# Performance work log

Measured on AMD Instinct MI355X. Metric: run time of the kernel, lower is better.

## Reference

```python
import jax, jax.numpy as jnp
import numpy as np

IMG = 224   # img_size
K = 8       # num_bands
E = 256     # embed_dim


def _radial_masks(size, k):
    # Faithful to torch _create_radial_masks: center = size//2, max_r = size/sqrt(2)
    center = size // 2
    y, x = jnp.meshgrid(jnp.arange(size), jnp.arange(size), indexing='ij')
    r = jnp.sqrt(((x - center) ** 2 + (y - center) ** 2).astype(jnp.float32))
    max_r = size / np.sqrt(2.0)
    step = np.float32(max_r / k)
    i = jnp.arange(k, dtype=jnp.float32)[:, None, None]
    masks = ((r[None] >= step * i) & (r[None] < step * (i + 1.0))).astype(jnp.float32)
    return masks  # [K, H, W]


def setup_inputs() -> dict:
    key = jax.random.key(0)
    ks = jax.random.split(key, 3)
    x = jax.random.normal(ks[0], (64, 3, IMG, IMG), dtype=jnp.float32)
    W1 = jax.random.normal(ks[1], (3, E), dtype=jnp.float32) * 0.3
    b1 = jnp.zeros((E,), jnp.float32)
    gamma = jnp.ones((E,), jnp.float32)
    beta = jnp.zeros((E,), jnp.float32)
    W2 = jax.random.normal(ks[2], (E, E), dtype=jnp.float32) * (1.0 / np.sqrt(E))
    b2 = jnp.zeros((E,), jnp.float32)
    return {"x": x, "W1": W1, "b1": b1, "gamma": gamma, "beta": beta, "W2": W2, "b2": b2}


def reference(x, W1, b1, gamma, beta, W2, b2):
    masks = _radial_masks(IMG, K)                    # [K,H,W], binary, non-overlapping
    x_gray = x.mean(axis=1)                          # [B,H,W]
    fft = jnp.fft.fftshift(jnp.fft.fft2(x_gray), axes=(-2, -1))
    mag = jnp.log1p(jnp.abs(fft))                    # log(1+|F|)
    mu = mag.mean(axis=(1, 2), keepdims=True)
    sd = jnp.std(mag, axis=(1, 2), keepdims=True, ddof=1) + 1e-6  # torch .std is unbiased
    magn = (mag - mu) / sd                           # [B,H,W]

    msum = masks.sum(axis=(1, 2))                    # [K], true mask pixel counts
    mask_sums = msum + 1e-6
    s1 = jnp.einsum('bhw,khw->bk', magn, masks)      # per-band sum
    s2 = jnp.einsum('bhw,khw->bk', magn * magn, masks)
    means = s1 / mask_sums
    # sum((magn - means)^2 * mask) = s2 - 2*means*s1 + means^2 * msum  (exact expansion)
    var_num = s2 - 2.0 * means * s1 + (means ** 2) * msum
    stds = jnp.sqrt(var_num / mask_sums + 1e-6)
    # masked_fill(mask==0, -1e9) then amax over H,W
    maxs = jnp.max(jnp.where(masks[None] > 0, magn[:, None], -1e9), axis=(2, 3))

    feats = jnp.stack([means, stds, maxs], axis=-1)  # [B,K,3]
    h = feats @ W1 + b1                              # [B,K,E]
    hm = h.mean(axis=-1, keepdims=True)
    hv = h.var(axis=-1, keepdims=True)
    h = (h - hm) / jnp.sqrt(hv + 1e-5) * gamma + beta  # LayerNorm, eps=1e-5
    h = jax.nn.relu(h)
    return h @ W2 + b2                               # [B,K,E]
```

## Files before the change

kernel.cpp:

```cpp
#include <hip/hip_runtime.h>
#include <math.h>

#define IMG 224
#define NPIX 50176
#define BATCH 64
#define EDIM 256

typedef _Float16 f16;
typedef __attribute__((ext_vector_type(8))) _Float16 f16x8;
typedef __attribute__((ext_vector_type(4))) _Float16 f16x4;
typedef __attribute__((ext_vector_type(4))) float f32x4;
typedef unsigned int u32;


__global__ __launch_bounds__(256) void gemmA_kernel(const float* __restrict__ x,
                                                    f16* __restrict__ B2t,
                                                    f16* __restrict__ W2h,
                                                    u32* __restrict__ statsz) {
  __shared__ float T[224];
  __shared__ f16 As[2][32][64];
  __shared__ f16 Bs[2][256][64];
  int m0 = blockIdx.x * 32;
  int tid = threadIdx.x;
  int lane = tid & 63, wid = tid >> 6;

  if (blockIdx.x == 0) {
#pragma unroll
    for (int i = 0; i < 9; ++i) {
      int idx = i * 256 + tid;
      if (idx < 2176) statsz[idx] = 0u;
    }
  }

  int arow = tid >> 3;
  int aseg = tid & 7;
  int am = m0 + arow;
  int ab = am / 224, ah = am - ab * 224;
  const float* px = x + (size_t)ab * 3 * NPIX + ah * IMG;
  int s0 = aseg ^ (arow & 7);

  f32x4 xlA[3][2], xlB[3][2];
  f32x4 acc[2][4];
#pragma unroll
  for (int i = 0; i < 2; ++i)
#pragma unroll
    for (int j = 0; j < 4; ++j) acc[i][j] = (f32x4){0.f, 0.f, 0.f, 0.f};

  auto issueA = [&](f32x4 (&xl)[3][2], int t) {
    int kb = t * 64 + aseg * 8;
    if (kb < 224) {
#pragma unroll
      for (int c = 0; c < 3; ++c) {
        xl[c][0] = *(const f32x4*)(px + c * NPIX + kb);
        xl[c][1] = *(const f32x4*)(px + c * NPIX + kb + 4);
      }
    }
  };
  auto writeA = [&](f32x4 (&xl)[3][2], int t, int bufi) {
    int kb = t * 64 + aseg * 8;
    f16x8 h0;
    if (kb < 224) {
#pragma unroll
      for (int j = 0; j < 8; ++j) {
        int q = j >> 2, r = j & 3;
        h0[j] = (f16)((xl[0][q][r] + xl[1][q][r] + xl[2][q][r]) * (1.0f / 3.0f));
      }
    } else {
#pragma unroll
      for (int j = 0; j < 8; ++j) h0[j] = (f16)0.f;
    }
    *(f16x8*)&As[bufi][arow][s0 * 8] = h0;
  };
  auto computeB = [&](int bufi, int t) {
    int row = tid;
    int v = (row < 113) ? row : row - 113;
    u32 off = (row < 113) ? 0u : 56u;
    u32 idx0 = ((u32)(t * 64) * (u32)v + off) % 224u;
    u32 idxm = (idx0 >= (u32)v) ? idx0 - (u32)v : idx0 + 224u - (u32)v;
    float cur = T[idx0];
    float prev = T[idxm];
    float k2c = 2.0f * T[v];
#pragma unroll
    for (int g = 0; g < 8; ++g) {
      f16x8 hv;
#pragma unroll
      for (int j = 0; j < 8; ++j) {
        hv[j] = (f16)cur;
        float nxt = __builtin_fmaf(k2c, cur, -prev);
        prev = cur; cur = nxt;
      }
      *(f16x8*)&Bs[bufi][row][(g ^ (row & 7)) * 8] = hv;
    }
  };
  auto mfmaStep = [&](int bufi) {
#pragma unroll
    for (int kk = 0; kk < 2; ++kk) {
      f16x8 af[2], bfr[4];
#pragma unroll
      for (int mi = 0; mi < 2; ++mi) {
        int row = mi * 16 + (lane & 15);
        int slot = (kk * 4 + (lane >> 4)) ^ (row & 7);
        af[mi] = *(const f16x8*)&As[bufi][row][slot * 8];
      }
#pragma unroll
      for (int nj = 0; nj < 4; ++nj) {
        int row = wid * 64 + nj * 16 + (lane & 15);
        int slot = (kk * 4 + (lane >> 4)) ^ (row & 7);
        bfr[nj] = *(const f16x8*)&Bs[bufi][row][slot * 8];
      }
#pragma unroll
      for (int mi = 0; mi < 2; ++mi)
#pragma unroll
        for (int nj = 0; nj < 4; ++nj)
          acc[mi][nj] = __builtin_amdgcn_mfma_f32_16x16x32_f16(
              af[mi], bfr[nj], acc[mi][nj], 0, 0, 0);
    }
  };

  issueA(xlA, 0);
  if (tid < 224) T[tid] = cospif((float)tid / 112.0f);
  issueA(xlB, 1);
  __syncthreads();
  computeB(0, 0);

  asm volatile("s_waitcnt vmcnt(6)" ::: "memory");
  writeA(xlA, 0, 0);
  asm volatile("s_waitcnt lgkmcnt(0)" ::: "memory");
  __builtin_amdgcn_s_barrier();
  issueA(xlA, 2);
  computeB(1, 1);
  mfmaStep(0);
  __builtin_amdgcn_s_barrier();
  asm volatile("s_waitcnt vmcnt(6)" ::: "memory");
  writeA(xlB, 1, 1);
  asm volatile("s_waitcnt lgkmcnt(0)" ::: "memory");
  __builtin_amdgcn_s_barrier();
  issueA(xlB, 3);
  computeB(0, 2);
  mfmaStep(1);
  __builtin_amdgcn_s_barrier();
  asm volatile("s_waitcnt vmcnt(6)" ::: "memory");
  writeA(xlA, 2, 0);
  asm volatile("s_waitcnt lgkmcnt(0)" ::: "memory");
  __builtin_amdgcn_s_barrier();
  computeB(1, 3);
  mfmaStep(0);
  __builtin_amdgcn_s_barrier();
  asm volatile("s_waitcnt vmcnt(0)" ::: "memory");
  writeA(xlB, 3, 1);
  asm volatile("s_waitcnt lgkmcnt(0)" ::: "memory");
  __builtin_amdgcn_s_barrier();
  mfmaStep(1);

  int nbase = wid * 64;
#pragma unroll
  for (int mi = 0; mi < 2; ++mi) {
#pragma unroll
    for (int nj = 0; nj < 4; ++nj) {
      int c = nbase + nj * 16 + (lane & 15);
      if (c >= 226) continue;
      int m = m0 + mi * 16 + ((lane >> 4) << 2);
      int b = m / 224;
      int h = m - b * 224;
      int v = c, kb = h;
      if (c >= 113) { v = c - 113; kb = 224 + h; }
      size_t off = (size_t)(b * 128 + v) * 448 + kb;
      f32x4 y = acc[mi][nj];
      f16x4 hv;
#pragma unroll
      for (int r = 0; r < 4; ++r) hv[r] = (f16)y[r];
      *(f16x4*)&B2t[off] = hv;
    }
  }

  {
    int r = blockIdx.x;
    int u = r >> 1;
    bool imrow = r & 1;
#pragma unroll
    for (int pass = 0; pass < 2; ++pass) {
      int k = pass * 256 + tid;
      if (k < 448) {
        bool kim = k >= 224;
        int kk = kim ? k - 224 : k;
        int m = (u * kk) % 224;
        float mf = (float)m / 112.0f;
        float c = cospif(mf), s = sinpif(mf);
        float val = imrow ? (kim ? c : -s) : (kim ? s : c);
        W2h[(size_t)r * 448 + k] = (f16)val;
      }
    }
  }
}

__global__ __launch_bounds__(256) void gemmB_kernel(const f16* __restrict__ W2h,
                                                    const f16* __restrict__ B2t,
                                                    float* __restrict__ stats) {
  __shared__ f16 As[64][64];
  __shared__ f16 Bs[128][64];
  int b = blockIdx.x;
  int m0 = blockIdx.y * 64;
  int tid = threadIdx.x;
  int lane = tid & 63, wid = tid >> 6;
  int wr = wid >> 1, wc = wid & 1;
  const f16* Ap = W2h + (size_t)m0 * 448;
  const f16* Bp = B2t + (size_t)b * 128 * 448;

  int srow = lane >> 3;
  int sk8 = (lane & 7) ^ srow;

  f32x4 acc[2][4];
#pragma unroll
  for (int i = 0; i < 2; ++i)
#pragma unroll
    for (int j = 0; j < 4; ++j) acc[i][j] = (f32x4){0.f, 0.f, 0.f, 0.f};

  auto stage_load = [&](f16x8 (&tmp)[6], int t) {
    int k0 = t * 64;
#pragma unroll
    for (int ci = 0; ci < 6; ++ci) {
      int c = wid * 6 + ci;
      const f16* src = (c < 8)
          ? Ap + (size_t)(c * 8 + srow) * 448 + k0 + sk8 * 8
          : Bp + (size_t)((c - 8) * 8 + srow) * 448 + k0 + sk8 * 8;
      tmp[ci] = *(const f16x8*)src;
    }
  };
  auto stage_write = [&](f16x8 (&tmp)[6]) {
#pragma unroll
    for (int ci = 0; ci < 6; ++ci) {
      int c = wid * 6 + ci;
      f16* dst = (c < 8) ? (&As[0][0] + c * 512 + lane * 8)
                         : (&Bs[0][0] + (c - 8) * 512 + lane * 8);
      *(f16x8*)dst = tmp[ci];
    }
  };
  auto mfmaStep = [&]() {
#pragma unroll
    for (int kk = 0; kk < 2; ++kk) {
      f16x8 af[2], bfr[4];
#pragma unroll
      for (int mi = 0; mi < 2; ++mi) {
        int row = wr * 32 + mi * 16 + (lane & 15);
        int slot = (kk * 4 + (lane >> 4)) ^ (row & 7);
        af[mi] = *(const f16x8*)&As[row][slot * 8];
      }
#pragma unroll
      for (int nj = 0; nj < 4; ++nj) {
        int row = wc * 64 + nj * 16 + (lane & 15);
        int slot = (kk * 4 + (lane >> 4)) ^ (row & 7);
        bfr[nj] = *(const f16x8*)&Bs[row][slot * 8];
      }
#pragma unroll
      for (int mi = 0; mi < 2; ++mi)
#pragma unroll
        for (int nj = 0; nj < 4; ++nj)
          acc[mi][nj] = __builtin_amdgcn_mfma_f32_16x16x32_f16(
              af[mi], bfr[nj], acc[mi][nj], 0, 0, 0);
    }
  };
  auto step = [&](f16x8 (&curT)[6], f16x8 (&nxtT)[6], int t, bool last) {
    stage_write(curT);
    __syncthreads();
    if (!last) stage_load(nxtT, t + 1);
    mfmaStep();
    __syncthreads();
  };

  f16x8 tA[6], tB[6];
  stage_load(tA, 0);
  step(tA, tB, 0, false);
  step(tB, tA, 1, false);
  step(tA, tB, 2, false);
  step(tB, tA, 3, false);
  step(tA, tB, 4, false);
  step(tB, tA, 5, false);
  step(tA, tA, 6, true);

  int rbase = m0 + wr * 32;
  const float step_ = (float)(158.39191898578665 / 8.0);
  float gsum = 0.f, gsq = 0.f;
  float s1[8] = {0}, s2[8] = {0}, cnt[8] = {0};
  float mx[8] = {0, 0, 0, 0, 0, 0, 0, 0};

#pragma unroll
  for (int mi = 0; mi < 2; ++mi) {
#pragma unroll
    for (int nj = 0; nj < 4; ++nj) {
      int n = wc * 64 + nj * 16 + (lane & 15);
      if (n >= 113) continue;
      float wgt = (n >= 1 && n <= 111) ? 2.f : 1.f;
      float dx2 = (float)(n * n);
      int rr = rbase + mi * 16 + ((lane >> 4) << 2);
      f32x4 f = acc[mi][nj];
#pragma unroll
      for (int p = 0; p < 2; ++p) {
        int u = (rr >> 1) + p;
        float re = f[2 * p], im = f[2 * p + 1];
        float mv = log1pf(sqrtf(re * re + im * im));
        int a = (u <= 111) ? u : 224 - u;
        float r = sqrtf((float)(a * a) + dx2);
        int bd = 255;
#pragma unroll
        for (int k = 0; k < 8; k++) {
          float lo = step_ * (float)k;
          float hi = step_ * (float)(k + 1);
          if (r >= lo && r < hi) bd = k;
        }
        float wm = wgt * mv;
        gsum += wm;
        gsq += wm * mv;
#pragma unroll
        for (int k = 0; k < 8; k++) {
          bool m = (bd == k);
          s1[k] += m ? wm : 0.f;
          s2[k] += m ? wm * mv : 0.f;
          cnt[k] += m ? wgt : 0.f;
          mx[k] = m ? fmaxf(mx[k], mv) : mx[k];
        }
      }
    }
  }

  float vals[34];
  vals[0] = gsum; vals[1] = gsq;
#pragma unroll
  for (int k = 0; k < 8; k++) {
    vals[2 + k] = s1[k]; vals[10 + k] = s2[k]; vals[18 + k] = mx[k]; vals[26 + k] = cnt[k];
  }
#pragma unroll
  for (int i = 0; i < 34; i++) {
    float v = vals[i];
    const bool isMax = (i >= 18 && i < 26);
#pragma unroll
    for (int off = 32; off > 0; off >>= 1) {
      float o = __shfl_down(v, off);
      v = isMax ? fmaxf(v, o) : (v + o);
    }
    vals[i] = v;
  }
  float* red = (float*)&As[0][0];
  if ((tid & 63) == 0) {
#pragma unroll
    for (int i = 0; i < 34; i++) red[wid * 34 + i] = vals[i];
  }
  __syncthreads();
  if (tid < 34) {
    bool isMax = (tid >= 18 && tid < 26);
    float v = red[tid];
#pragma unroll
    for (int ww = 1; ww < 4; ww++) {
      float o = red[ww * 34 + tid];
      v = isMax ? fmaxf(v, o) : (v + o);
    }
    if (isMax)
      atomicMax((u32*)&stats[b * 34 + tid], __float_as_uint(v));
    else
      atomicAdd(&stats[b * 34 + tid], v);
  }
}

__global__ __launch_bounds__(256) void mlp_kernel(const float* __restrict__ stats,
                                                  const float* __restrict__ W1,
                                                  const float* __restrict__ b1,
                                                  const float* __restrict__ gamma,
                                                  const float* __restrict__ beta,
                                                  const float* __restrict__ W2m,
                                                  const float* __restrict__ b2,
                                                  float* __restrict__ out) {
  int blk = blockIdx.x;
  int b = blk >> 2;
  int k0 = (blk & 3) * 2;
  int e = threadIdx.x;
  int lane = e & 63, wave = e >> 6;

  __shared__ float st[34];
  if (e < 34) st[e] = stats[b * 34 + e];
  __syncthreads();

  const float N = (float)NPIX;
  float mu = st[0] / N;
  float varg = fmaxf(st[1] - N * mu * mu, 0.0f) / (N - 1.0f);
  float sd = sqrtf(varg) + 1e-6f;

  float g_e = gamma[e], bt_e = beta[e], b1_e = b1[e];
  float w1a = W1[e], w1b = W1[EDIM + e], w1c = W1[2 * EDIM + e];

  float h[2];
#pragma unroll
  for (int q = 0; q < 2; ++q) {
    int k = k0 + q;
    float s1r = st[2 + k], s2r = st[10 + k], mxr = st[18 + k], cntk = st[26 + k];
    float ms = cntk + 1e-6f;
    float s1n = (s1r - mu * cntk) / sd;
    float s2n = (s2r - 2.0f * mu * s1r + mu * mu * cntk) / (sd * sd);
    float mean_k = s1n / ms;
    float var_num = s2n - 2.0f * mean_k * s1n + mean_k * mean_k * cntk;
    float std_k = sqrtf(var_num / ms + 1e-6f);
    float max_k = (mxr - mu) / sd;
    h[q] = mean_k * w1a + std_k * w1b + max_k * w1c + b1_e;
  }

  float v4[4] = {h[0], h[0] * h[0], h[1], h[1] * h[1]};
#pragma unroll
  for (int i = 0; i < 4; ++i) {
#pragma unroll
    for (int off = 32; off > 0; off >>= 1) v4[i] += __shfl_down(v4[i], off);
  }
  __shared__ float red[4][4];
  __shared__ float mm[4];
  if (lane == 0) {
#pragma unroll
    for (int i = 0; i < 4; ++i) red[wave][i] = v4[i];
  }
  __syncthreads();
  if (e == 0) {
#pragma unroll
    for (int i = 0; i < 4; ++i) {
      float t = red[0][i] + red[1][i] + red[2][i] + red[3][i];
      red[0][i] = t;
    }
    float hm0 = red[0][0] / 256.0f, hm1 = red[0][2] / 256.0f;
    mm[0] = hm0;
    mm[1] = fmaxf(red[0][1] / 256.0f - hm0 * hm0, 0.0f);
    mm[2] = hm1;
    mm[3] = fmaxf(red[0][3] / 256.0f - hm1 * hm1, 0.0f);
  }
  __syncthreads();

  __shared__ float hsT[EDIM][2];
#pragma unroll
  for (int q = 0; q < 2; ++q) {
    float hn = (h[q] - mm[2 * q]) / sqrtf(mm[2 * q + 1] + 1e-5f) * g_e + bt_e;
    hsT[e][q] = fmaxf(hn, 0.0f);
  }
  __syncthreads();

  float a0 = b2[e], a1 = a0;
#pragma unroll 8
  for (int j = 0; j < EDIM; j++) {
    float w = W2m[j * EDIM + e];
    float2 hp = *(const float2*)&hsT[j][0];
    a0 += hp.x * w;
    a1 += hp.y * w;
  }
  out[(size_t)(b * 8 + k0) * EDIM + e] = a0;
  out[(size_t)(b * 8 + k0 + 1) * EDIM + e] = a1;
}

extern "C" void kernel_launch(void* const* d_in, const int* in_sizes, int n_in,
                              void* d_out, int out_size, void* d_ws, size_t ws_size,
                              hipStream_t stream) {
  const float* x     = (const float*)d_in[0];
  const float* W1    = (const float*)d_in[1];
  const float* b1    = (const float*)d_in[2];
  const float* gamma = (const float*)d_in[3];
  const float* beta  = (const float*)d_in[4];
  const float* W2m   = (const float*)d_in[5];
  const float* b2    = (const float*)d_in[6];
  float* out = (float*)d_out;

  char* W = (char*)d_ws;
  f16* B2t = (f16*)W;
  float* stats = (float*)(W + 7340032);
  f16* W2h = (f16*)(W + 7340032 + 8704);

  gemmA_kernel<<<dim3(448), dim3(256), 0, stream>>>(x, B2t, W2h, (u32*)stats);
  gemmB_kernel<<<dim3(BATCH, 7), dim3(256), 0, stream>>>(W2h, B2t, stats);
  mlp_kernel<<<dim3(256), dim3(256), 0, stream>>>(stats, W1, b1, gamma, beta, W2m, b2, out);
}
```

Measured before the change: 50.93 us.

## Split band statistics out of GEMM epilogue into separate stats kernel

The GEMM-B epilogue now only writes log-magnitude values to a workspace buffer. A new stats kernel computes per-band sums, squares, counts and maxima over chunks and writes per-chunk partials, which the MLP kernel reduces. This removes the heavy register-bound binning epilogue and the global atomics, along with the stats zeroing in gemmA. The cost is an extra launch and about 6.5 MB of extra global write and read traffic.

```diff
diff --git a/kernel.cpp b/kernel.cpp
--- a/kernel.cpp
+++ b/kernel.cpp
@@ -15,22 +15,13 @@
 
 __global__ __launch_bounds__(256) void gemmA_kernel(const float* __restrict__ x,
                                                     f16* __restrict__ B2t,
-                                                    f16* __restrict__ W2h,
-                                                    u32* __restrict__ statsz) {
+                                                    f16* __restrict__ W2h) {
   __shared__ float T[224];
   __shared__ f16 As[2][32][64];
   __shared__ f16 Bs[2][256][64];
   int m0 = blockIdx.x * 32;
   int tid = threadIdx.x;
   int lane = tid & 63, wid = tid >> 6;
-
-  if (blockIdx.x == 0) {
-#pragma unroll
-    for (int i = 0; i < 9; ++i) {
-      int idx = i * 256 + tid;
-      if (idx < 2176) statsz[idx] = 0u;
-    }
-  }
 
   int arow = tid >> 3;
   int aseg = tid & 7;
@@ -195,7 +186,7 @@
 
 __global__ __launch_bounds__(256) void gemmB_kernel(const f16* __restrict__ W2h,
                                                     const f16* __restrict__ B2t,
-                                                    float* __restrict__ stats) {
+                                                    float* __restrict__ magc) {
   __shared__ f16 As[64][64];
   __shared__ f16 Bs[128][64];
   int b = blockIdx.x;
@@ -278,19 +269,12 @@
   step(tA, tA, 6, true);
 
   int rbase = m0 + wr * 32;
-  const float step_ = (float)(158.39191898578665 / 8.0);
-  float gsum = 0.f, gsq = 0.f;
-  float s1[8] = {0}, s2[8] = {0}, cnt[8] = {0};
-  float mx[8] = {0, 0, 0, 0, 0, 0, 0, 0};
-
 #pragma unroll
   for (int mi = 0; mi < 2; ++mi) {
 #pragma unroll
     for (int nj = 0; nj < 4; ++nj) {
       int n = wc * 64 + nj * 16 + (lane & 15);
       if (n >= 113) continue;
-      float wgt = (n >= 1 && n <= 111) ? 2.f : 1.f;
-      float dx2 = (float)(n * n);
       int rr = rbase + mi * 16 + ((lane >> 4) << 2);
       f32x4 f = acc[mi][nj];
 #pragma unroll
@@ -298,26 +282,53 @@
         int u = (rr >> 1) + p;
         float re = f[2 * p], im = f[2 * p + 1];
         float mv = log1pf(sqrtf(re * re + im * im));
-        int a = (u <= 111) ? u : 224 - u;
-        float r = sqrtf((float)(a * a) + dx2);
-        int bd = 255;
-#pragma unroll
-        for (int k = 0; k < 8; k++) {
-          float lo = step_ * (float)k;
-          float hi = step_ * (float)(k + 1);
-          if (r >= lo && r < hi) bd = k;
-        }
-        float wm = wgt * mv;
-        gsum += wm;
-        gsq += wm * mv;
-#pragma unroll
-        for (int k = 0; k < 8; k++) {
-          bool m = (bd == k);
-          s1[k] += m ? wm : 0.f;
-          s2[k] += m ? wm * mv : 0.f;
-          cnt[k] += m ? wgt : 0.f;
-          mx[k] = m ? fmaxf(mx[k], mv) : mx[k];
-        }
+        magc[((size_t)b * 224 + u) * 113 + n] = mv;
+      }
+    }
+  }
+}
+
+__global__ __launch_bounds__(256) void stats_kernel(const float* __restrict__ magc,
+                                                    float* __restrict__ part) {
+  int chunk = blockIdx.x;
+  int b = blockIdx.y;
+  int tid = threadIdx.x;
+  const float* mb = magc + (size_t)b * 25312 + chunk * 1808;
+  int pbase = chunk * 1808;
+  const float step = (float)(158.39191898578665 / 8.0);
+
+  float gsum = 0.f, gsq = 0.f;
+  float s1[8] = {0}, s2[8] = {0}, cnt[8] = {0};
+  float mx[8] = {0, 0, 0, 0, 0, 0, 0, 0};
+
+#pragma unroll
+  for (int i = 0; i < 8; ++i) {
+    int off = i * 256 + tid;
+    if (off < 1808) {
+      float v = mb[off];
+      int p = pbase + off;
+      int uu = p / 113;
+      int vv = p - uu * 113;
+      float wgt = (vv >= 1 && vv <= 111) ? 2.f : 1.f;
+      int a = (uu <= 111) ? uu : 224 - uu;
+      float r = sqrtf((float)(a * a + vv * vv));
+      int bd = 255;
+#pragma unroll
+      for (int k = 0; k < 8; k++) {
+        float lo = step * (float)k;
+        float hi = step * (float)(k + 1);
+        if (r >= lo && r < hi) bd = k;
+      }
+      float wm = wgt * v;
+      gsum += wm;
+      gsq += wm * v;
+#pragma unroll
+      for (int k = 0; k < 8; k++) {
+        bool m = (bd == k);
+        s1[k] += m ? wm : 0.f;
+        s2[k] += m ? wm * v : 0.f;
+        cnt[k] += m ? wgt : 0.f;
+        mx[k] = m ? fmaxf(mx[k], v) : mx[k];
       }
     }
   }
@@ -339,28 +350,26 @@
     }
     vals[i] = v;
   }
-  float* red = (float*)&As[0][0];
+  __shared__ float red[4][34];
+  int w = tid >> 6;
   if ((tid & 63) == 0) {
 #pragma unroll
-    for (int i = 0; i < 34; i++) red[wid * 34 + i] = vals[i];
+    for (int i = 0; i < 34; i++) red[w][i] = vals[i];
   }
   __syncthreads();
   if (tid < 34) {
     bool isMax = (tid >= 18 && tid < 26);
-    float v = red[tid];
+    float v = red[0][tid];
 #pragma unroll
     for (int ww = 1; ww < 4; ww++) {
-      float o = red[ww * 34 + tid];
+      float o = red[ww][tid];
       v = isMax ? fmaxf(v, o) : (v + o);
     }
-    if (isMax)
-      atomicMax((u32*)&stats[b * 34 + tid], __float_as_uint(v));
-    else
-      atomicAdd(&stats[b * 34 + tid], v);
+    part[((size_t)b * 14 + chunk) * 34 + tid] = v;
   }
 }
 
-__global__ __launch_bounds__(256) void mlp_kernel(const float* __restrict__ stats,
+__global__ __launch_bounds__(256) void mlp_kernel(const float* __restrict__ part,
                                                   const float* __restrict__ W1,
                                                   const float* __restrict__ b1,
                                                   const float* __restrict__ gamma,
@@ -375,7 +384,17 @@
   int lane = e & 63, wave = e >> 6;
 
   __shared__ float st[34];
-  if (e < 34) st[e] = stats[b * 34 + e];
+  if (e < 34) {
+    bool isMax = (e >= 18 && e < 26);
+    const float* pb = part + (size_t)b * 14 * 34;
+    float v = pb[e];
+#pragma unroll
+    for (int c = 1; c < 14; c++) {
+      float o = pb[c * 34 + e];
+      v = isMax ? fmaxf(v, o) : (v + o);
+    }
+    st[e] = v;
+  }
   __syncthreads();
 
   const float N = (float)NPIX;
@@ -462,10 +481,12 @@
 
   char* W = (char*)d_ws;
   f16* B2t = (f16*)W;
-  float* stats = (float*)(W + 7340032);
-  f16* W2h = (f16*)(W + 7340032 + 8704);
-
-  gemmA_kernel<<<dim3(448), dim3(256), 0, stream>>>(x, B2t, W2h, (u32*)stats);
-  gemmB_kernel<<<dim3(BATCH, 7), dim3(256), 0, stream>>>(W2h, B2t, stats);
-  mlp_kernel<<<dim3(256), dim3(256), 0, stream>>>(stats, W1, b1, gamma, beta, W2m, b2, out);
+  f16* W2h = (f16*)(W + 7340032);
+  float* magc = (float*)(W + 7741440);
+  float* part = (float*)(W + 14213632);
+
+  gemmA_kernel<<<dim3(448), dim3(256), 0, stream>>>(x, B2t, W2h);
+  gemmB_kernel<<<dim3(BATCH, 7), dim3(256), 0, stream>>>(W2h, B2t, magc);
+  stats_kernel<<<dim3(14, BATCH), dim3(256), 0, stream>>>(magc, part);
+  mlp_kernel<<<dim3(256), dim3(256), 0, stream>>>(part, W1, b1, gamma, beta, W2m, b2, out);
 }
```

Result: slower. 55.96 us (+9.9%).
